# Optimization experiments

Hardware: AMD Instinct MI355X
Metric: run time of the kernel (lower is better)

The kernel has to match this reference:

```python
import jax, jax.numpy as jnp
import numpy as np

B, T, L, E = 4, 256, 128, 64  # batch, sample_size (frames), num_harmonies, embedding_size


def setup_inputs() -> dict:
    key = jax.random.key(0)
    k1, k2 = jax.random.split(key)
    return {
        "note_embedding": jax.random.normal(k1, (B, T, E), dtype=jnp.float32),
        "harmony_embedding": jax.random.normal(k2, (B, L, E), dtype=jnp.float32),
    }


def reference(note_embedding, harmony_embedding):
    """SegmentScore.forward: for every segment [s, e] (s <= e), attend the harmony
    embeddings (queries, [B,L,E]) over the note embeddings in that segment
    (keys/values) with scaled dot-product softmax, then score = <harmony, attended>.
    Equivalent closed form: score[b,s,e,l] =
        sum_{t=s..e} softmax_t(raw[b,l,s:e+1])[t] * dot[b,l,t]
    where dot = <harmony_l, note_t> and raw = dot / sqrt(E).
    Vectorized via cumulative sums over the end index for each start index.
    Output: [B, T, T, L]; entries with e < s are 0 (matching torch zeros init).
    """
    scale = 1.0 / jnp.sqrt(jnp.asarray(E, note_embedding.dtype))
    dot = jnp.einsum("ble,bte->blt", harmony_embedding, note_embedding)  # [B,L,T]
    raw = dot * scale
    t_idx = jnp.arange(T)

    def body(carry, s):
        valid = t_idx >= s                                  # [T]
        masked = jnp.where(valid, raw, -jnp.inf)            # [B,L,T]
        m = jnp.max(masked, axis=-1, keepdims=True)         # stable softmax max over t>=s
        exps = jnp.exp(masked - m)                          # 0 where invalid
        denom = jnp.cumsum(exps, axis=-1)                   # running normalizer over e
        numer = jnp.cumsum(exps * dot, axis=-1)             # running <harmony, attended>
        row = jnp.where(valid, numer / jnp.maximum(denom, 1e-30), 0.0)  # [B,L,T_e]
        return carry, row

    _, rows = jax.lax.scan(body, None, t_idx)               # [T_s, B, L, T_e]
    return jnp.transpose(rows, (1, 0, 3, 2))                # [B, T_s, T_e, L]
```

## Files before the change

kernel.cpp:

```cpp
#include <hip/hip_runtime.h>
#include <hip/hip_bf16.h>

#define BB 4
#define TT 256
#define LL 128
#define EE 64
#define SCALE 0.125f

__global__ __launch_bounds__(256) void k_prefix(const float* __restrict__ note,
                                                const float* __restrict__ harm,
                                                double2* __restrict__ P) {
    int b = blockIdx.x >> 7;
    int l = blockIdx.x & 127;
    int t = threadIdx.x;

    __shared__ __align__(16) float h[EE];
    if (t < EE) h[t] = harm[(b * LL + l) * EE + t];
    __syncthreads();

    const float4* n4 = (const float4*)(note + (b * TT + t) * EE);
    const float4* h4 = (const float4*)h;
    float acc = 0.f;
#pragma unroll
    for (int i = 0; i < EE / 4; ++i) {
        float4 nv = n4[i];
        float4 hv = h4[i];
        acc += nv.x * hv.x + nv.y * hv.y + nv.z * hv.z + nv.w * hv.w;
    }
    float dot = acc;
    float raw = dot * SCALE;

    __shared__ float red[256];
    red[t] = raw;
    __syncthreads();
#pragma unroll
    for (int off = 128; off > 0; off >>= 1) {
        if (t < off) red[t] = fmaxf(red[t], red[t + off]);
        __syncthreads();
    }
    float M = red[0];
    __syncthreads();

    float ex = __expf(raw - M);
    double vd = (double)ex;
    double vn = (double)ex * (double)dot;

    __shared__ double sd[TT], sn[TT];
    sd[t] = vd;
    sn[t] = vn;
    __syncthreads();
#pragma unroll
    for (int off = 1; off < TT; off <<= 1) {
        double pd = 0.0, pn = 0.0;
        if (t >= off) { pd = sd[t - off]; pn = sn[t - off]; }
        __syncthreads();
        vd += pd;
        vn += pn;
        sd[t] = vd;
        sn[t] = vn;
        __syncthreads();
    }

    P[(b * TT + t) * LL + l] = make_double2(vd, vn);
}

__global__ __launch_bounds__(256) void k_out(const double2* __restrict__ P,
                                             float* __restrict__ out) {
    int blk = blockIdx.x;
    int et = blk & 31;
    int s  = (blk >> 5) & 255;
    int b  = blk >> 13;
    int l  = threadIdx.x & 127;
    int eo = threadIdx.x >> 7;

    double2 Ps = make_double2(0.0, 0.0);
    if (s > 0) Ps = P[(b * TT + (s - 1)) * LL + l];

    int e0 = et * 8 + eo * 4;
    float* op = out + (size_t)(((b * TT + s) * TT) + e0) * LL + l;
    const double2* pp = P + (b * TT + e0) * LL + l;

#pragma unroll
    for (int k = 0; k < 4; ++k) {
        int e = e0 + k;
        float r = 0.f;
        if (e >= s) {
            double2 Pe = pp[k * LL];
            float den = (float)(Pe.x - Ps.x);
            float num = (float)(Pe.y - Ps.y);
            r = __fdividef(num, fmaxf(den, 1e-30f));
        }
        op[k * LL] = r;
    }
}

extern "C" void kernel_launch(void* const* d_in, const int* in_sizes, int n_in,
                              void* d_out, int out_size, void* d_ws, size_t ws_size,
                              hipStream_t stream) {
    const float* note = (const float*)d_in[0];
    const float* harm = (const float*)d_in[1];
    float* out = (float*)d_out;

    double2* P = (double2*)d_ws;

    k_prefix<<<BB * LL, 256, 0, stream>>>(note, harm, P);
    k_out<<<BB * TT * 32, 256, 0, stream>>>(P, out);
}
```

Measured before the change: 153.6 us.

## Use wave shuffles for prefix scan and tile output kernel over start rows

New measurement: 152.1 us. No clear change (-1.0%).

```diff
diff --git a/kernel.cpp b/kernel.cpp
--- a/kernel.cpp
+++ b/kernel.cpp
@@ -13,6 +13,8 @@
     int b = blockIdx.x >> 7;
     int l = blockIdx.x & 127;
     int t = threadIdx.x;
+    int lane = t & 63;
+    int wave = t >> 6;
 
     __shared__ __align__(16) float h[EE];
     if (t < EE) h[t] = harm[(b * LL + l) * EE + t];
@@ -30,36 +32,34 @@
     float dot = acc;
     float raw = dot * SCALE;
 
-    __shared__ float red[256];
-    red[t] = raw;
+    float m = raw;
+#pragma unroll
+    for (int off = 32; off > 0; off >>= 1) m = fmaxf(m, __shfl_xor(m, off));
+    __shared__ float wmax[4];
+    if (lane == 0) wmax[wave] = m;
     __syncthreads();
-#pragma unroll
-    for (int off = 128; off > 0; off >>= 1) {
-        if (t < off) red[t] = fmaxf(red[t], red[t + off]);
-        __syncthreads();
-    }
-    float M = red[0];
-    __syncthreads();
+    float M = fmaxf(fmaxf(wmax[0], wmax[1]), fmaxf(wmax[2], wmax[3]));
 
     float ex = __expf(raw - M);
     double vd = (double)ex;
     double vn = (double)ex * (double)dot;
 
-    __shared__ double sd[TT], sn[TT];
-    sd[t] = vd;
-    sn[t] = vn;
+#pragma unroll
+    for (int off = 1; off < 64; off <<= 1) {
+        double od = __shfl_up(vd, off);
+        double on = __shfl_up(vn, off);
+        if (lane >= off) { vd += od; vn += on; }
+    }
+    __shared__ double wtd[4], wtn[4];
+    if (lane == 63) { wtd[wave] = vd; wtn[wave] = vn; }
     __syncthreads();
+    double od = 0.0, on = 0.0;
 #pragma unroll
-    for (int off = 1; off < TT; off <<= 1) {
-        double pd = 0.0, pn = 0.0;
-        if (t >= off) { pd = sd[t - off]; pn = sn[t - off]; }
-        __syncthreads();
-        vd += pd;
-        vn += pn;
-        sd[t] = vd;
-        sn[t] = vn;
-        __syncthreads();
+    for (int w = 0; w < 3; ++w) {
+        if (w < wave) { od += wtd[w]; on += wtn[w]; }
     }
+    vd += od;
+    vn += on;
 
     P[(b * TT + t) * LL + l] = make_double2(vd, vn);
 }
@@ -67,30 +67,44 @@
 __global__ __launch_bounds__(256) void k_out(const double2* __restrict__ P,
                                              float* __restrict__ out) {
     int blk = blockIdx.x;
-    int et = blk & 31;
-    int s  = (blk >> 5) & 255;
-    int b  = blk >> 13;
+    int eq = blk & 3;
+    int st = (blk >> 2) & 63;
+    int b  = blk >> 8;
     int l  = threadIdx.x & 127;
     int eo = threadIdx.x >> 7;
+    int s0 = st * 4;
+    int e_begin = eq * 64 + eo * 32;
 
-    double2 Ps = make_double2(0.0, 0.0);
-    if (s > 0) Ps = P[(b * TT + (s - 1)) * LL + l];
-
-    int e0 = et * 8 + eo * 4;
-    float* op = out + (size_t)(((b * TT + s) * TT) + e0) * LL + l;
-    const double2* pp = P + (b * TT + e0) * LL + l;
-
+    double2 Ps[4];
 #pragma unroll
     for (int k = 0; k < 4; ++k) {
-        int e = e0 + k;
-        float r = 0.f;
-        if (e >= s) {
-            double2 Pe = pp[k * LL];
-            float den = (float)(Pe.x - Ps.x);
-            float num = (float)(Pe.y - Ps.y);
-            r = __fdividef(num, fmaxf(den, 1e-30f));
+        int s = s0 + k;
+        Ps[k] = (s > 0) ? P[(b * TT + s - 1) * LL + l] : make_double2(0.0, 0.0);
+    }
+
+    const double2* pp = P + (b * TT + e_begin) * LL + l;
+    float* op = out + ((size_t)(b * TT + s0) * TT + e_begin) * LL + l;
+    const int srow = TT * LL;
+
+#pragma unroll 4
+    for (int ke = 0; ke < 32; ++ke) {
+        int e = e_begin + ke;
+        if (e < s0) {
+#pragma unroll
+            for (int k = 0; k < 4; ++k) op[k * srow + ke * LL] = 0.f;
+        } else {
+            double2 Pe = pp[ke * LL];
+#pragma unroll
+            for (int k = 0; k < 4; ++k) {
+                float r = 0.f;
+                if (e >= s0 + k) {
+                    float den = (float)(Pe.x - Ps[k].x);
+                    float num = (float)(Pe.y - Ps[k].y);
+                    r = __fdividef(num, fmaxf(den, 1e-30f));
+                }
+                op[k * srow + ke * LL] = r;
+            }
         }
-        op[k * LL] = r;
     }
 }
 
@@ -104,5 +118,5 @@
     double2* P = (double2*)d_ws;
 
     k_prefix<<<BB * LL, 256, 0, stream>>>(note, harm, P);
-    k_out<<<BB * TT * 32, 256, 0, stream>>>(P, out);
+    k_out<<<BB * 64 * 4, 256, 0, stream>>>(P, out);
 }
```
